# Optimization experiments

Hardware: AMD Instinct MI355X
Metric: run time of the kernel (lower is better)

## Reference

```python
import jax, jax.numpy as jnp
import numpy as np

B, D, T, K = 32768, 1024, 100, 4  # batch, input_dim, num_trees, 2**(tree_depth-1)

def setup_inputs() -> dict:
    key = jax.random.key(0)
    k1, k2, k3, k4, k5 = jax.random.split(key, 5)
    s1 = 1.0 / np.sqrt(D)
    s2 = 1.0 / np.sqrt(K)
    return {
        "x": jax.random.normal(k1, (B, D), dtype=jnp.float32),
        "W1": jax.random.uniform(k2, (T, K, D), jnp.float32, -s1, s1),  # per-tree first Linear
        "b1": jax.random.uniform(k3, (T, K), jnp.float32, -s1, s1),
        "final_weight": jnp.full((T,), 1.0 / T, dtype=jnp.float32),
        "fc_w": jax.random.uniform(k4, (2, K), jnp.float32, -s2, s2),
        "fc_b": jax.random.uniform(k5, (2,), jnp.float32, -s2, s2),
    }

def reference(x, W1, b1, final_weight, fc_w, fc_b):
    # split_probs for all trees at once: [B, T, K]
    split = jnp.einsum("bd,tkd->btk", x, W1) + b1[None, :, :]
    leaf = jax.nn.sigmoid(split)  # tree[1] is Sigmoid applied to split_probs
    # sum(split.unsqueeze(1)*leaf.unsqueeze(2), -1) == leaf * sum_k(split)
    tree_out = leaf * jnp.sum(split, axis=-1, keepdims=True)  # [B, T, K]
    weighted = jnp.einsum("btk,t->bk", tree_out, final_weight)  # [B, K]
    logits = weighted @ fc_w.T + fc_b  # [B, 2]
    return logits
```

## Files before the change

### kernel.cpp

```cpp
#include <hip/hip_runtime.h>
#include <hip/hip_bf16.h>


typedef __bf16 bf16x8 __attribute__((ext_vector_type(8)));
typedef float f32x4 __attribute__((ext_vector_type(4)));

#define B_ROWS 32768
#define D_DIM  1024
#define N_COLS 400
#define NPAD   448
#define BM     128
#define BK     64
#define NCHUNK 16
#define THREADS 512
#define NTPW 7
#define MT   4

__device__ __forceinline__ unsigned short f2bf(float f) {
    unsigned int u = __float_as_uint(f);
    u += 0x7FFFu + ((u >> 16) & 1u);
    return (unsigned short)(u >> 16);
}
__device__ __forceinline__ unsigned int pk2(float a, float b) {
    return (unsigned int)f2bf(a) | ((unsigned int)f2bf(b) << 16);
}
__device__ __forceinline__ uint4 cvt8u(float4 a, float4 b) {
    uint4 u;
    u.x = pk2(a.x, a.y); u.y = pk2(a.z, a.w);
    u.z = pk2(b.x, b.y); u.w = pk2(b.z, b.w);
    return u;
}
__device__ __forceinline__ bf16x8 cvt8(float4 a, float4 b) {
    return __builtin_bit_cast(bf16x8, cvt8u(a, b));
}

__global__ void cvt_pad_bf16_kernel(const float* __restrict__ in,
                                    unsigned short* __restrict__ out) {
    size_t i = ((size_t)blockIdx.x * 256 + threadIdx.x) * 8;
    if (i < (size_t)N_COLS * D_DIM) {
        float4 v0 = *reinterpret_cast<const float4*>(in + i);
        float4 v1 = *reinterpret_cast<const float4*>(in + i + 4);
        *reinterpret_cast<uint4*>(out + i) = cvt8u(v0, v1);
    } else {
        uint4 z; z.x = z.y = z.z = z.w = 0u;
        *reinterpret_cast<uint4*>(out + i) = z;
    }
}

__device__ __forceinline__ void gl_lds16(const unsigned short* g,
                                         unsigned short* l) {
    __builtin_amdgcn_global_load_lds(
        (const __attribute__((address_space(1))) unsigned int*)g,
        (__attribute__((address_space(3))) unsigned int*)l,
        16, 0, 0);
}

#define FOR_N_(OP, m) OP(m,0) OP(m,1) OP(m,2) OP(m,3) OP(m,4) OP(m,5) OP(m,6)
#define FOR_MN(OP) FOR_N_(OP,0) FOR_N_(OP,1) FOR_N_(OP,2) FOR_N_(OP,3)

#define DECL_ACC(m,n) f32x4 acc##m##n = {};
#define MFMA_MN(m,n) acc##m##n = __builtin_amdgcn_mfma_f32_16x16x32_bf16( \
        afr##m, bfr##n, acc##m##n, 0, 0, 0);

template <int MODE>
__global__ __launch_bounds__(THREADS, 2) void xgb_v14(
    const float* __restrict__ x,
    const void*  __restrict__ b_any,
    const float* __restrict__ b1,
    const float* __restrict__ fw,
    const float* __restrict__ fcw,
    const float* __restrict__ fcb,
    float* __restrict__ out)
{
    __shared__ __align__(16) unsigned short Abuf[2][BM * BK];
    __shared__ __align__(16) unsigned short Bbuf[2][NPAD * BK];
    __shared__ float Pbuf[BM * 4 * 2];

    const int tid  = threadIdx.x;
    const int wave = tid >> 6;
    const int lane = tid & 63;
    const int quad = lane >> 4;
    const int l15  = lane & 15;
    const int mh   = wave >> 2;
    const int nf   = wave & 3;
    const int row0 = blockIdx.x * BM;

    FOR_MN(DECL_ACC)

    if (MODE == 0) {
        const unsigned short* w1b = (const unsigned short*)b_any;

#define BDECL(t) const unsigned short* bsrc##t; int bdst##t; \
        { const int s_ = wave + 8 * (t); const int rr_ = lane >> 3; \
          const int cc_ = ((lane & 7) - rr_) & 7; \
          bsrc##t = w1b + (size_t)(s_ * 8 + rr_) * D_DIM + cc_ * 8; \
          bdst##t = s_ * 512; }
        BDECL(0) BDECL(1) BDECL(2) BDECL(3) BDECL(4) BDECL(5) BDECL(6)

#define STAGEB(kc, Bb) do { \
        gl_lds16(bsrc0 + (kc), (Bb) + bdst0); \
        gl_lds16(bsrc1 + (kc), (Bb) + bdst1); \
        gl_lds16(bsrc2 + (kc), (Bb) + bdst2); \
        gl_lds16(bsrc3 + (kc), (Bb) + bdst3); \
        gl_lds16(bsrc4 + (kc), (Bb) + bdst4); \
        gl_lds16(bsrc5 + (kc), (Bb) + bdst5); \
        gl_lds16(bsrc6 + (kc), (Bb) + bdst6); } while (0)

        const int r0a = tid >> 3, c0a = tid & 7;
        const float* asrc0 = x + (size_t)(row0 + r0a) * D_DIM + c0a * 8;
        const float* asrc1 = asrc0 + (size_t)64 * D_DIM;
        const int adst0 = r0a * 64 + ((c0a + r0a) & 7) * 8;
        float4 aX0lo, aX0hi, aX1lo, aX1hi;
        float4 aY0lo, aY0hi, aY1lo, aY1hi;

#define LOADA_X(kc) do { \
        aX0lo = *reinterpret_cast<const float4*>(asrc0 + (kc));     \
        aX0hi = *reinterpret_cast<const float4*>(asrc0 + (kc) + 4); \
        aX1lo = *reinterpret_cast<const float4*>(asrc1 + (kc));     \
        aX1hi = *reinterpret_cast<const float4*>(asrc1 + (kc) + 4); } while (0)
#define LOADA_Y(kc) do { \
        aY0lo = *reinterpret_cast<const float4*>(asrc0 + (kc));     \
        aY0hi = *reinterpret_cast<const float4*>(asrc0 + (kc) + 4); \
        aY1lo = *reinterpret_cast<const float4*>(asrc1 + (kc));     \
        aY1hi = *reinterpret_cast<const float4*>(asrc1 + (kc) + 4); } while (0)
#define WRITEA_X(Ab) do { \
        *reinterpret_cast<uint4*>((Ab) + adst0)        = cvt8u(aX0lo, aX0hi); \
        *reinterpret_cast<uint4*>((Ab) + adst0 + 4096) = cvt8u(aX1lo, aX1hi); \
        } while (0)
#define WRITEA_Y(Ab) do { \
        *reinterpret_cast<uint4*>((Ab) + adst0)        = cvt8u(aY0lo, aY0hi); \
        *reinterpret_cast<uint4*>((Ab) + adst0 + 4096) = cvt8u(aY1lo, aY1hi); \
        } while (0)

#define LOAD_AFR(m) { const int row_ = mh * 64 + (m) * 16 + l15; \
        const int p_ = (quad + h * 4 + row_) & 7; \
        afr##m = *reinterpret_cast<const bf16x8*>(Ab_ + row_ * 64 + p_ * 8); }
#define LOAD_BFR(n) { const int row_ = (nf * NTPW + (n)) * 16 + l15; \
        const int p_ = (quad + h * 4 + row_) & 7; \
        bfr##n = *reinterpret_cast<const bf16x8*>(Bb_ + row_ * 64 + p_ * 8); }

        LOADA_X(0);
        WRITEA_X(Abuf[0]);
        STAGEB(0, Bbuf[0]);
        __builtin_amdgcn_sched_barrier(0);
        LOADA_Y(BK);

        #pragma unroll 1
        for (int c = 0; c < NCHUNK; ++c) {
            const int cur = c & 1;
            const unsigned short* Ab_ = Abuf[cur];
            const unsigned short* Bb_ = Bbuf[cur];
            if (c == NCHUNK - 1) {
                asm volatile("s_waitcnt vmcnt(0)" ::: "memory");
            } else {
                asm volatile("s_waitcnt vmcnt(4)" ::: "memory");
            }
            asm volatile("s_waitcnt lgkmcnt(0)" ::: "memory");
            __builtin_amdgcn_s_barrier();
            __builtin_amdgcn_sched_barrier(0);
            if (c + 1 < NCHUNK) {
                STAGEB((c + 1) * BK, Bbuf[1 - cur]);
                __builtin_amdgcn_sched_barrier(0);
                if (cur == 0) WRITEA_Y(Abuf[1]);
                else          WRITEA_X(Abuf[0]);
                if (c + 2 < NCHUNK) {
                    if (cur == 0) LOADA_X((c + 2) * BK);
                    else          LOADA_Y((c + 2) * BK);
                }
                __builtin_amdgcn_sched_barrier(0);
            }
            #pragma unroll
            for (int h = 0; h < 2; ++h) {
                bf16x8 afr0, afr1, afr2, afr3;
                bf16x8 bfr0, bfr1, bfr2, bfr3, bfr4, bfr5, bfr6;
                LOAD_AFR(0) LOAD_AFR(1) LOAD_AFR(2) LOAD_AFR(3)
                LOAD_BFR(0) LOAD_BFR(1) LOAD_BFR(2) LOAD_BFR(3)
                LOAD_BFR(4) LOAD_BFR(5) LOAD_BFR(6)
                FOR_MN(MFMA_MN)
            }
        }
    } else {
        const float* af = x + (size_t)(row0 + mh * 64 + l15) * D_DIM + quad * 8;
#define PBF(n) const float* pbf##n; { \
        int r_ = (nf * NTPW + (n)) * 16 + l15; if (r_ > N_COLS - 1) r_ = 0; \
        pbf##n = (const float*)b_any + (size_t)r_ * D_DIM + quad * 8; }
        PBF(0) PBF(1) PBF(2) PBF(3) PBF(4) PBF(5) PBF(6)
        for (int step = 0; step < 32; ++step) {
            const int off = step * 32;
            bf16x8 afr0, afr1, afr2, afr3;
            bf16x8 bfr0, bfr1, bfr2, bfr3, bfr4, bfr5, bfr6;
#define LAF2(m) afr##m = cvt8( \
            *reinterpret_cast<const float4*>(af + (size_t)(m) * 16 * D_DIM + off), \
            *reinterpret_cast<const float4*>(af + (size_t)(m) * 16 * D_DIM + off + 4));
#define LBF2(n) bfr##n = cvt8( \
            *reinterpret_cast<const float4*>(pbf##n + off), \
            *reinterpret_cast<const float4*>(pbf##n + off + 4));
            LAF2(0) LAF2(1) LAF2(2) LAF2(3)
            LBF2(0) LBF2(1) LBF2(2) LBF2(3) LBF2(4) LBF2(5) LBF2(6)
            FOR_MN(MFMA_MN)
        }
    }

    const float fcw0 = fcw[l15 & 3];
    const float fcw1 = fcw[4 + (l15 & 3)];

#define PRE_N(n) \
    const int  col##n  = (nf * NTPW + (n)) * 16 + l15; \
    const bool ok##n   = (col##n < N_COLS); \
    const float bias##n = ok##n ? b1[ok##n ? col##n : 0] : 0.0f; \
    const float tw##n   = ok##n ? fw[ok##n ? (col##n >> 2) : 0] : 0.0f;
    PRE_N(0) PRE_N(1) PRE_N(2) PRE_N(3) PRE_N(4) PRE_N(5) PRE_N(6)

#define EPI_TERM(m,r,n) { \
        const float split_ = acc##m##n[r] + bias##n; \
        float s_ = split_; \
        s_ += __shfl_xor(s_, 1); \
        s_ += __shfl_xor(s_, 2); \
        const float leaf_ = 1.0f / (1.0f + __expf(-split_)); \
        const float val_ = tw##n * leaf_ * s_; \
        q0 += val_ * fcw0; q1 += val_ * fcw1; }

#define EPI_ONE(m,r) { \
        float q0 = 0.f, q1 = 0.f; \
        EPI_TERM(m,r,0) EPI_TERM(m,r,1) EPI_TERM(m,r,2) EPI_TERM(m,r,3) \
        EPI_TERM(m,r,4) EPI_TERM(m,r,5) EPI_TERM(m,r,6) \
        q0 += __shfl_xor(q0, 1); q0 += __shfl_xor(q0, 2); \
        q0 += __shfl_xor(q0, 4); q0 += __shfl_xor(q0, 8); \
        q1 += __shfl_xor(q1, 1); q1 += __shfl_xor(q1, 2); \
        q1 += __shfl_xor(q1, 4); q1 += __shfl_xor(q1, 8); \
        const int row_ = mh * 64 + (m) * 16 + quad * 4 + (r);    \
        if (l15 == 0) Pbuf[(row_ * 4 + nf) * 2 + 0] = q0; \
        if (l15 == 1) Pbuf[(row_ * 4 + nf) * 2 + 1] = q1; }

#define EPI_M(m) EPI_ONE(m,0) EPI_ONE(m,1) EPI_ONE(m,2) EPI_ONE(m,3)
    EPI_M(0) EPI_M(1) EPI_M(2) EPI_M(3)

    __syncthreads();

    if (tid < 2 * BM) {
        const int r = tid >> 1, j = tid & 1;
        float s = fcb[j];
        #pragma unroll
        for (int w = 0; w < 4; ++w)
            s += Pbuf[(r * 4 + w) * 2 + j];
        out[(row0 + r) * 2 + j] = s;
    }
}

extern "C" void kernel_launch(void* const* d_in, const int* in_sizes, int n_in,
                              void* d_out, int out_size, void* d_ws, size_t ws_size,
                              hipStream_t stream) {
    const float* x   = (const float*)d_in[0];
    const float* W1  = (const float*)d_in[1];
    const float* b1  = (const float*)d_in[2];
    const float* fw  = (const float*)d_in[3];
    const float* fcw = (const float*)d_in[4];
    const float* fcb = (const float*)d_in[5];
    float* out = (float*)d_out;

    const size_t pad_elems = (size_t)NPAD * D_DIM;
    if (ws_size >= pad_elems * sizeof(unsigned short)) {
        unsigned short* w1b = (unsigned short*)d_ws;
        cvt_pad_bf16_kernel<<<(int)(pad_elems / 2048), 256, 0, stream>>>(W1, w1b);
        xgb_v14<0><<<B_ROWS / BM, THREADS, 0, stream>>>(
            x, (const void*)w1b, b1, fw, fcw, fcb, out);
    } else {
        xgb_v14<2><<<B_ROWS / BM, THREADS, 0, stream>>>(
            x, (const void*)W1, b1, fw, fcw, fcb, out);
    }
}
```

Before: 229.4 us.

## Deepen GEMM pipeline to four LDS slots with smaller K chunks

Replaces the double-buffered BK=64 pipeline with a four-slot ring of BK=32 chunks, prefetching three chunks ahead for both the x tile (global to registers, then converted to bf16) and the W1 tile (global_load_lds). Swizzles and per-wave staging are reworked for the 32-wide rows, and B staging now uses 7 waves with 4 loads each. The aim is to hide global memory latency with more loads in flight. The cost is twice as many barriers per K, more registers held for A prefetches, and the same LDS footprint.

```diff
diff --git a/kernel.cpp b/kernel.cpp
--- a/kernel.cpp
+++ b/kernel.cpp
@@ -10,8 +10,9 @@
 #define N_COLS 400
 #define NPAD   448
 #define BM     128
-#define BK     64
-#define NCHUNK 16
+#define BK     32
+#define NCHUNK 32
+#define NSLOT  4
 #define THREADS 512
 #define NTPW 7
 #define MT   4
@@ -63,7 +64,7 @@
         afr##m, bfr##n, acc##m##n, 0, 0, 0);
 
 template <int MODE>
-__global__ __launch_bounds__(THREADS, 2) void xgb_v14(
+__global__ __launch_bounds__(THREADS, 2) void xgb_v18(
     const float* __restrict__ x,
     const void*  __restrict__ b_any,
     const float* __restrict__ b1,
@@ -72,8 +73,8 @@
     const float* __restrict__ fcb,
     float* __restrict__ out)
 {
-    __shared__ __align__(16) unsigned short Abuf[2][BM * BK];
-    __shared__ __align__(16) unsigned short Bbuf[2][NPAD * BK];
+    __shared__ __align__(16) unsigned short Aslot[NSLOT][BM * BK];
+    __shared__ __align__(16) unsigned short Bslot[NSLOT][NPAD * BK];
     __shared__ float Pbuf[BM * 4 * 2];
 
     const int tid  = threadIdx.x;
@@ -91,93 +92,91 @@
         const unsigned short* w1b = (const unsigned short*)b_any;
 
 #define BDECL(t) const unsigned short* bsrc##t; int bdst##t; \
-        { const int s_ = wave + 8 * (t); const int rr_ = lane >> 3; \
-          const int cc_ = ((lane & 7) - rr_) & 7; \
-          bsrc##t = w1b + (size_t)(s_ * 8 + rr_) * D_DIM + cc_ * 8; \
+        { const int s_ = wave + 7 * (t); \
+          const int rb_ = s_ * 16 + (lane >> 2); \
+          const int cc_ = ((lane & 3) - (rb_ >> 1)) & 3; \
+          bsrc##t = w1b + (size_t)rb_ * D_DIM + cc_ * 8; \
           bdst##t = s_ * 512; }
-        BDECL(0) BDECL(1) BDECL(2) BDECL(3) BDECL(4) BDECL(5) BDECL(6)
-
-#define STAGEB(kc, Bb) do { \
+        BDECL(0) BDECL(1) BDECL(2) BDECL(3)
+
+#define STAGEB(kc, Bb) do { if (wave < 7) { \
         gl_lds16(bsrc0 + (kc), (Bb) + bdst0); \
         gl_lds16(bsrc1 + (kc), (Bb) + bdst1); \
         gl_lds16(bsrc2 + (kc), (Bb) + bdst2); \
-        gl_lds16(bsrc3 + (kc), (Bb) + bdst3); \
-        gl_lds16(bsrc4 + (kc), (Bb) + bdst4); \
-        gl_lds16(bsrc5 + (kc), (Bb) + bdst5); \
-        gl_lds16(bsrc6 + (kc), (Bb) + bdst6); } while (0)
-
-        const int r0a = tid >> 3, c0a = tid & 7;
-        const float* asrc0 = x + (size_t)(row0 + r0a) * D_DIM + c0a * 8;
-        const float* asrc1 = asrc0 + (size_t)64 * D_DIM;
-        const int adst0 = r0a * 64 + ((c0a + r0a) & 7) * 8;
-        float4 aX0lo, aX0hi, aX1lo, aX1hi;
-        float4 aY0lo, aY0hi, aY1lo, aY1hi;
-
-#define LOADA_X(kc) do { \
-        aX0lo = *reinterpret_cast<const float4*>(asrc0 + (kc));     \
-        aX0hi = *reinterpret_cast<const float4*>(asrc0 + (kc) + 4); \
-        aX1lo = *reinterpret_cast<const float4*>(asrc1 + (kc));     \
-        aX1hi = *reinterpret_cast<const float4*>(asrc1 + (kc) + 4); } while (0)
-#define LOADA_Y(kc) do { \
-        aY0lo = *reinterpret_cast<const float4*>(asrc0 + (kc));     \
-        aY0hi = *reinterpret_cast<const float4*>(asrc0 + (kc) + 4); \
-        aY1lo = *reinterpret_cast<const float4*>(asrc1 + (kc));     \
-        aY1hi = *reinterpret_cast<const float4*>(asrc1 + (kc) + 4); } while (0)
-#define WRITEA_X(Ab) do { \
-        *reinterpret_cast<uint4*>((Ab) + adst0)        = cvt8u(aX0lo, aX0hi); \
-        *reinterpret_cast<uint4*>((Ab) + adst0 + 4096) = cvt8u(aX1lo, aX1hi); \
-        } while (0)
-#define WRITEA_Y(Ab) do { \
-        *reinterpret_cast<uint4*>((Ab) + adst0)        = cvt8u(aY0lo, aY0hi); \
-        *reinterpret_cast<uint4*>((Ab) + adst0 + 4096) = cvt8u(aY1lo, aY1hi); \
+        gl_lds16(bsrc3 + (kc), (Bb) + bdst3); } } while (0)
+
+        const int r0a = tid >> 2, c0a = tid & 3;
+        const float* asrc = x + (size_t)(row0 + r0a) * D_DIM + c0a * 8;
+        const int adst = r0a * 32 + ((c0a + (r0a >> 1)) & 3) * 8;
+        float4 aR0a, aR0b, aR1a, aR1b, aR2a, aR2b, aR3a, aR3b;
+
+#define LOADA(S, kc) do { \
+        aR##S##a = *reinterpret_cast<const float4*>(asrc + (kc));     \
+        aR##S##b = *reinterpret_cast<const float4*>(asrc + (kc) + 4); } while (0)
+#define WRITEA(S, Ab) do { \
+        *reinterpret_cast<uint4*>((Ab) + adst) = cvt8u(aR##S##a, aR##S##b); \
         } while (0)
 
 #define LOAD_AFR(m) { const int row_ = mh * 64 + (m) * 16 + l15; \
-        const int p_ = (quad + h * 4 + row_) & 7; \
-        afr##m = *reinterpret_cast<const bf16x8*>(Ab_ + row_ * 64 + p_ * 8); }
+        const int p_ = (quad + (row_ >> 1)) & 3; \
+        afr##m = *reinterpret_cast<const bf16x8*>(Ab_ + row_ * 32 + p_ * 8); }
 #define LOAD_BFR(n) { const int row_ = (nf * NTPW + (n)) * 16 + l15; \
-        const int p_ = (quad + h * 4 + row_) & 7; \
-        bfr##n = *reinterpret_cast<const bf16x8*>(Bb_ + row_ * 64 + p_ * 8); }
-
-        LOADA_X(0);
-        WRITEA_X(Abuf[0]);
-        STAGEB(0, Bbuf[0]);
+        const int p_ = (quad + (row_ >> 1)) & 3; \
+        bfr##n = *reinterpret_cast<const bf16x8*>(Bb_ + row_ * 32 + p_ * 8); }
+
+#define COMPUTE(PH) do { \
+        const unsigned short* Ab_ = Aslot[PH]; \
+        const unsigned short* Bb_ = Bslot[PH]; \
+        bf16x8 afr0, afr1, afr2, afr3; \
+        bf16x8 bfr0, bfr1, bfr2, bfr3, bfr4, bfr5, bfr6; \
+        LOAD_AFR(0) LOAD_AFR(1) LOAD_AFR(2) LOAD_AFR(3) \
+        LOAD_BFR(0) LOAD_BFR(1) LOAD_BFR(2) LOAD_BFR(3) \
+        LOAD_BFR(4) LOAD_BFR(5) LOAD_BFR(6) \
+        FOR_MN(MFMA_MN) \
+        } while (0)
+
+#define VMWAIT(c_) do { \
+        if ((c_) <= NCHUNK - 3) { \
+            if (wave < 7) asm volatile("s_waitcnt vmcnt(12)" ::: "memory"); \
+            else          asm volatile("s_waitcnt vmcnt(4)"  ::: "memory"); \
+        } else if ((c_) == NCHUNK - 2) { \
+            if (wave < 7) asm volatile("s_waitcnt vmcnt(6)" ::: "memory"); \
+            else          asm volatile("s_waitcnt vmcnt(2)" ::: "memory"); \
+        } else { \
+            asm volatile("s_waitcnt vmcnt(0)" ::: "memory"); \
+        } \
+        __builtin_amdgcn_sched_barrier(0); \
+        } while (0)
+
+#define CHUNK_BODY(PH, PH3, cc) do { \
+        const int c_ = (cc) + (PH); \
+        VMWAIT(c_); \
+        WRITEA(PH, Aslot[PH]); \
+        asm volatile("s_waitcnt lgkmcnt(0)" ::: "memory"); \
+        __builtin_amdgcn_s_barrier(); \
+        __builtin_amdgcn_sched_barrier(0); \
+        if (c_ + 3 < NCHUNK) { \
+            const int kc3_ = (c_ + 3) * BK; \
+            STAGEB(kc3_, Bslot[PH3]); \
+            LOADA(PH3, kc3_); \
+        } \
+        __builtin_amdgcn_sched_barrier(0); \
+        COMPUTE(PH); \
+        } while (0)
+
+        STAGEB(0, Bslot[0]);  LOADA(0, 0);
         __builtin_amdgcn_sched_barrier(0);
-        LOADA_Y(BK);
+        STAGEB(BK, Bslot[1]); LOADA(1, BK);
+        __builtin_amdgcn_sched_barrier(0);
+        STAGEB(2 * BK, Bslot[2]); LOADA(2, 2 * BK);
+        __builtin_amdgcn_sched_barrier(0);
 
         #pragma unroll 1
-        for (int c = 0; c < NCHUNK; ++c) {
-            const int cur = c & 1;
-            const unsigned short* Ab_ = Abuf[cur];
-            const unsigned short* Bb_ = Bbuf[cur];
-            if (c == NCHUNK - 1) {
-                asm volatile("s_waitcnt vmcnt(0)" ::: "memory");
-            } else {
-                asm volatile("s_waitcnt vmcnt(4)" ::: "memory");
-            }
-            asm volatile("s_waitcnt lgkmcnt(0)" ::: "memory");
-            __builtin_amdgcn_s_barrier();
-            __builtin_amdgcn_sched_barrier(0);
-            if (c + 1 < NCHUNK) {
-                STAGEB((c + 1) * BK, Bbuf[1 - cur]);
-                __builtin_amdgcn_sched_barrier(0);
-                if (cur == 0) WRITEA_Y(Abuf[1]);
-                else          WRITEA_X(Abuf[0]);
-                if (c + 2 < NCHUNK) {
-                    if (cur == 0) LOADA_X((c + 2) * BK);
-                    else          LOADA_Y((c + 2) * BK);
-                }
-                __builtin_amdgcn_sched_barrier(0);
-            }
-            #pragma unroll
-            for (int h = 0; h < 2; ++h) {
-                bf16x8 afr0, afr1, afr2, afr3;
-                bf16x8 bfr0, bfr1, bfr2, bfr3, bfr4, bfr5, bfr6;
-                LOAD_AFR(0) LOAD_AFR(1) LOAD_AFR(2) LOAD_AFR(3)
-                LOAD_BFR(0) LOAD_BFR(1) LOAD_BFR(2) LOAD_BFR(3)
-                LOAD_BFR(4) LOAD_BFR(5) LOAD_BFR(6)
-                FOR_MN(MFMA_MN)
-            }
+        for (int cc = 0; cc < NCHUNK; cc += 4) {
+            CHUNK_BODY(0, 3, cc);
+            CHUNK_BODY(1, 0, cc);
+            CHUNK_BODY(2, 1, cc);
+            CHUNK_BODY(3, 2, cc);
         }
     } else {
         const float* af = x + (size_t)(row0 + mh * 64 + l15) * D_DIM + quad * 8;
@@ -243,7 +242,7 @@
         #pragma unroll
         for (int w = 0; w < 4; ++w)
             s += Pbuf[(r * 4 + w) * 2 + j];
-        out[(row0 + r) * 2 + j] = s;
+        out[(size_t)(row0 + r) * 2 + j] = s;
     }
 }
 
@@ -262,10 +261,10 @@
     if (ws_size >= pad_elems * sizeof(unsigned short)) {
         unsigned short* w1b = (unsigned short*)d_ws;
         cvt_pad_bf16_kernel<<<(int)(pad_elems / 2048), 256, 0, stream>>>(W1, w1b);
-        xgb_v14<0><<<B_ROWS / BM, THREADS, 0, stream>>>(
+        xgb_v18<0><<<B_ROWS / BM, THREADS, 0, stream>>>(
             x, (const void*)w1b, b1, fw, fcw, fcb, out);
     } else {
-        xgb_v14<2><<<B_ROWS / BM, THREADS, 0, stream>>>(
+        xgb_v18<2><<<B_ROWS / BM, THREADS, 0, stream>>>(
             x, (const void*)W1, b1, fw, fcw, fcb, out);
     }
 }
```

Measured after the change: 240.5 us. 4.8% more time.

## Split K-chunk into two phases interleaving B staging with MFMA, raise MFMA priority

Applied to the files above, without the earlier changes.

The main loop now runs the two k-halves as separate phases. Half of the next chunk's B tile is issued into LDS after the first-half fragment loads, and the rest, plus the A tile writes and the next A global loads, after the second-half fragment loads. Each phase ends with its own workgroup barrier and LDS wait, and the MFMA block is wrapped in s_setprio to favour matrix issue. The goal is to spread memory traffic across the compute so it hides better behind MFMAs, at the cost of an extra barrier per chunk.

```diff
diff --git a/kernel.cpp b/kernel.cpp
--- a/kernel.cpp
+++ b/kernel.cpp
@@ -63,7 +63,7 @@
         afr##m, bfr##n, acc##m##n, 0, 0, 0);
 
 template <int MODE>
-__global__ __launch_bounds__(THREADS, 2) void xgb_v14(
+__global__ __launch_bounds__(THREADS, 2) void xgb_v20(
     const float* __restrict__ x,
     const void*  __restrict__ b_any,
     const float* __restrict__ b1,
@@ -97,11 +97,12 @@
           bdst##t = s_ * 512; }
         BDECL(0) BDECL(1) BDECL(2) BDECL(3) BDECL(4) BDECL(5) BDECL(6)
 
-#define STAGEB(kc, Bb) do { \
+#define STAGEB_P0(kc, Bb) do { \
         gl_lds16(bsrc0 + (kc), (Bb) + bdst0); \
         gl_lds16(bsrc1 + (kc), (Bb) + bdst1); \
         gl_lds16(bsrc2 + (kc), (Bb) + bdst2); \
-        gl_lds16(bsrc3 + (kc), (Bb) + bdst3); \
+        gl_lds16(bsrc3 + (kc), (Bb) + bdst3); } while (0)
+#define STAGEB_P1(kc, Bb) do { \
         gl_lds16(bsrc4 + (kc), (Bb) + bdst4); \
         gl_lds16(bsrc5 + (kc), (Bb) + bdst5); \
         gl_lds16(bsrc6 + (kc), (Bb) + bdst6); } while (0)
@@ -132,51 +133,74 @@
         *reinterpret_cast<uint4*>((Ab) + adst0 + 4096) = cvt8u(aY1lo, aY1hi); \
         } while (0)
 
-#define LOAD_AFR(m) { const int row_ = mh * 64 + (m) * 16 + l15; \
-        const int p_ = (quad + h * 4 + row_) & 7; \
+#define LOAD_AFR(m, H) { const int row_ = mh * 64 + (m) * 16 + l15; \
+        const int p_ = (quad + (H) * 4 + row_) & 7; \
         afr##m = *reinterpret_cast<const bf16x8*>(Ab_ + row_ * 64 + p_ * 8); }
-#define LOAD_BFR(n) { const int row_ = (nf * NTPW + (n)) * 16 + l15; \
-        const int p_ = (quad + h * 4 + row_) & 7; \
+#define LOAD_BFR(n, H) { const int row_ = (nf * NTPW + (n)) * 16 + l15; \
+        const int p_ = (quad + (H) * 4 + row_) & 7; \
         bfr##n = *reinterpret_cast<const bf16x8*>(Bb_ + row_ * 64 + p_ * 8); }
 
         LOADA_X(0);
         WRITEA_X(Abuf[0]);
-        STAGEB(0, Bbuf[0]);
+        __builtin_amdgcn_sched_barrier(0);
+        STAGEB_P0(0, Bbuf[0]);
+        STAGEB_P1(0, Bbuf[0]);
         __builtin_amdgcn_sched_barrier(0);
         LOADA_Y(BK);
+        asm volatile("s_waitcnt lgkmcnt(0)" ::: "memory");
+        __builtin_amdgcn_sched_barrier(0);
 
         #pragma unroll 1
         for (int c = 0; c < NCHUNK; ++c) {
             const int cur = c & 1;
             const unsigned short* Ab_ = Abuf[cur];
             const unsigned short* Bb_ = Bbuf[cur];
-            if (c == NCHUNK - 1) {
+            const int kc1 = (c + 1) * BK;
+            if (c <= NCHUNK - 2) {
+                asm volatile("s_waitcnt vmcnt(4)" ::: "memory");
+            } else {
                 asm volatile("s_waitcnt vmcnt(0)" ::: "memory");
-            } else {
-                asm volatile("s_waitcnt vmcnt(4)" ::: "memory");
             }
-            asm volatile("s_waitcnt lgkmcnt(0)" ::: "memory");
+            __builtin_amdgcn_sched_barrier(0);
             __builtin_amdgcn_s_barrier();
             __builtin_amdgcn_sched_barrier(0);
-            if (c + 1 < NCHUNK) {
-                STAGEB((c + 1) * BK, Bbuf[1 - cur]);
-                __builtin_amdgcn_sched_barrier(0);
-                if (cur == 0) WRITEA_Y(Abuf[1]);
-                else          WRITEA_X(Abuf[0]);
+            {
+                bf16x8 afr0, afr1, afr2, afr3;
+                bf16x8 bfr0, bfr1, bfr2, bfr3, bfr4, bfr5, bfr6;
+                LOAD_AFR(0, 0) LOAD_AFR(1, 0) LOAD_AFR(2, 0) LOAD_AFR(3, 0)
+                LOAD_BFR(0, 0) LOAD_BFR(1, 0) LOAD_BFR(2, 0) LOAD_BFR(3, 0)
+                LOAD_BFR(4, 0) LOAD_BFR(5, 0) LOAD_BFR(6, 0)
+                if (c + 1 < NCHUNK) STAGEB_P0(kc1, Bbuf[1 - cur]);
+                __builtin_amdgcn_sched_barrier(0);
+                __builtin_amdgcn_s_barrier();
+                asm volatile("s_waitcnt lgkmcnt(0)" ::: "memory");
+                __builtin_amdgcn_sched_barrier(0);
+                __builtin_amdgcn_s_setprio(1);
+                FOR_MN(MFMA_MN)
+                __builtin_amdgcn_s_setprio(0);
+            }
+            {
+                bf16x8 afr0, afr1, afr2, afr3;
+                bf16x8 bfr0, bfr1, bfr2, bfr3, bfr4, bfr5, bfr6;
+                LOAD_AFR(0, 1) LOAD_AFR(1, 1) LOAD_AFR(2, 1) LOAD_AFR(3, 1)
+                LOAD_BFR(0, 1) LOAD_BFR(1, 1) LOAD_BFR(2, 1) LOAD_BFR(3, 1)
+                LOAD_BFR(4, 1) LOAD_BFR(5, 1) LOAD_BFR(6, 1)
+                if (c + 1 < NCHUNK) {
+                    STAGEB_P1(kc1, Bbuf[1 - cur]);
+                    if (cur == 0) WRITEA_Y(Abuf[1]);
+                    else          WRITEA_X(Abuf[0]);
+                }
                 if (c + 2 < NCHUNK) {
                     if (cur == 0) LOADA_X((c + 2) * BK);
                     else          LOADA_Y((c + 2) * BK);
                 }
                 __builtin_amdgcn_sched_barrier(0);
-            }
-            #pragma unroll
-            for (int h = 0; h < 2; ++h) {
-                bf16x8 afr0, afr1, afr2, afr3;
-                bf16x8 bfr0, bfr1, bfr2, bfr3, bfr4, bfr5, bfr6;
-                LOAD_AFR(0) LOAD_AFR(1) LOAD_AFR(2) LOAD_AFR(3)
-                LOAD_BFR(0) LOAD_BFR(1) LOAD_BFR(2) LOAD_BFR(3)
-                LOAD_BFR(4) LOAD_BFR(5) LOAD_BFR(6)
+                __builtin_amdgcn_s_barrier();
+                asm volatile("s_waitcnt lgkmcnt(0)" ::: "memory");
+                __builtin_amdgcn_sched_barrier(0);
+                __builtin_amdgcn_s_setprio(1);
                 FOR_MN(MFMA_MN)
+                __builtin_amdgcn_s_setprio(0);
             }
         }
     } else {
@@ -243,7 +267,7 @@
         #pragma unroll
         for (int w = 0; w < 4; ++w)
             s += Pbuf[(r * 4 + w) * 2 + j];
-        out[(row0 + r) * 2 + j] = s;
+        out[(size_t)(row0 + r) * 2 + j] = s;
     }
 }
 
@@ -262,10 +286,10 @@
     if (ws_size >= pad_elems * sizeof(unsigned short)) {
         unsigned short* w1b = (unsigned short*)d_ws;
         cvt_pad_bf16_kernel<<<(int)(pad_elems / 2048), 256, 0, stream>>>(W1, w1b);
-        xgb_v14<0><<<B_ROWS / BM, THREADS, 0, stream>>>(
+        xgb_v20<0><<<B_ROWS / BM, THREADS, 0, stream>>>(
             x, (const void*)w1b, b1, fw, fcw, fcb, out);
     } else {
-        xgb_v14<2><<<B_ROWS / BM, THREADS, 0, stream>>>(
+        xgb_v20<2><<<B_ROWS / BM, THREADS, 0, stream>>>(
             x, (const void*)W1, b1, fw, fcw, fcb, out);
     }
 }
```

After: 231.4 us. Within noise of the previous version (+0.9%).
